# Performance work log

Measured on AMD Instinct MI355X. Metric: run time of the kernel, lower is better.

The kernel has to match this reference:

```python
import jax, jax.numpy as jnp
import numpy as np

B, N, C = 4, 2047, 1024
H = 16
D = C // H  # head_dim = 64
SCALE = D ** -0.5


def setup_inputs() -> dict:
    key = jax.random.key(0)
    ks = jax.random.split(key, 5)
    return {
        "x": jax.random.normal(ks[0], (B, N, C), dtype=jnp.float32),
        "qkv_w": jax.random.normal(ks[1], (3 * C, C), dtype=jnp.float32) * (C ** -0.5),
        "proj_w": jax.random.normal(ks[2], (C, C), dtype=jnp.float32) * (C ** -0.5),
        "proj_b": jax.random.normal(ks[3], (C,), dtype=jnp.float32) * 0.02,
        "bias": jax.random.normal(ks[4], (H, N, N), dtype=jnp.float32) * 0.02,
    }


def reference(x, qkv_w, proj_w, proj_b, bias):
    b, n, c = x.shape
    qkv = (x @ qkv_w.T).reshape(b, n, 3, H, D)
    qkv = jnp.transpose(qkv, (2, 0, 3, 1, 4))
    q, k, v = qkv[0], qkv[1], qkv[2]
    q = q * SCALE
    # scores (B,H,N,N) + additive relative-position bias (H,N,N)
    attn = jnp.einsum('bhnd,bhmd->bhnm', q, k) + bias[None]
    attn = jax.nn.softmax(attn, axis=-1)
    out = jnp.einsum('bhnm,bhmd->bhnd', attn, v)
    out = jnp.transpose(out, (0, 2, 1, 3)).reshape(b, n, c)
    return out @ proj_w.T + proj_b
```

## Files before the change

### kernel.cpp

```cpp
#include <hip/hip_runtime.h>
#include <hip/hip_bf16.h>

typedef __bf16 bf16;
typedef __attribute__((ext_vector_type(8))) __bf16 bf16x8;
typedef __attribute__((ext_vector_type(4))) __bf16 bf16x4;
typedef __attribute__((ext_vector_type(4))) float f32x4;

#define MFMA16(a, b, c) __builtin_amdgcn_mfma_f32_16x16x32_bf16((a), (b), (c), 0, 0, 0)

constexpr int Bb = 4, Nn = 2047, Cc = 1024, Hh = 16, Dd = 64;
constexpr int M_ROWS = Bb * Nn;
constexpr int NPAD = 2048;
constexpr float SCALE = 0.125f;
constexpr float NEG_BIG = -1e30f;

__device__ inline bf16x8 bzero8() {
    bf16x8 v;
    for (int i = 0; i < 8; ++i) v[i] = (bf16)0.0f;
    return v;
}
__device__ inline bf16x8 bones8() {
    bf16x8 v;
    for (int i = 0; i < 8; ++i) v[i] = (bf16)1.0f;
    return v;
}
__device__ inline f32x4 fzero4() {
    f32x4 v = {0.f, 0.f, 0.f, 0.f};
    return v;
}

__device__ __forceinline__ void async_copy16(const void* g, void* l) {
    __builtin_amdgcn_global_load_lds(
        (const __attribute__((address_space(1))) unsigned int*)g,
        (__attribute__((address_space(3))) unsigned int*)l, 16, 0, 0);
}

__global__ __launch_bounds__(256) void cvt3_kernel(
    const float* __restrict__ a, bf16* __restrict__ oa, int na8,
    const float* __restrict__ b, bf16* __restrict__ ob, int nb8,
    const float* __restrict__ c, bf16* __restrict__ oc, int nc8) {
    int i = blockIdx.x * blockDim.x + threadIdx.x;
    const float* src;
    bf16* dst;
    int j = i;
    if (j < na8) {
        src = a; dst = oa;
    } else {
        j -= na8;
        if (j < nb8) {
            src = b; dst = ob;
        } else {
            j -= nb8;
            if (j >= nc8) return;
            src = c; dst = oc;
        }
    }
    float4 x0 = ((const float4*)src)[2 * (size_t)j];
    float4 x1 = ((const float4*)src)[2 * (size_t)j + 1];
    bf16x8 v;
    v[0] = (bf16)x0.x; v[1] = (bf16)x0.y; v[2] = (bf16)x0.z; v[3] = (bf16)x0.w;
    v[4] = (bf16)x1.x; v[5] = (bf16)x1.y; v[6] = (bf16)x1.z; v[7] = (bf16)x1.w;
    *(bf16x8*)(dst + 8 * (size_t)j) = v;
}

__global__ __launch_bounds__(256) void transpose_v_kernel(
    const bf16* __restrict__ vd, bf16* __restrict__ vtd) {
    __shared__ bf16 t[64 * 72];
    const int bh = blockIdx.x, nt = blockIdx.y;
    const int tid = threadIdx.x;
    const bf16* src = vd + (size_t)bh * Nn * Dd;
    bf16* dst = vtd + (size_t)bh * Dd * NPAD;
    int c = tid;
    for (int it = 0; it < 2; ++it, c += 256) {
        int row = c >> 3, d8 = (c & 7) * 8;
        int gn = nt * 64 + row;
        bf16x8 v = bzero8();
        if (gn < Nn) v = *(const bf16x8*)(src + (size_t)gn * Dd + d8);
        *(bf16x8*)(t + row * 72 + d8) = v;
    }
    __syncthreads();
    c = tid;
    for (int it = 0; it < 2; ++it, c += 256) {
        int d = c >> 3, j8 = (c & 7) * 8;
        bf16x8 v;
        for (int k = 0; k < 8; ++k) v[k] = t[(j8 + k) * 72 + d];
        *(bf16x8*)(dst + (size_t)d * NPAD + nt * 64 + j8) = v;
    }
}

template <int NOUT, int MODE>
__global__ __launch_bounds__(256, 2) void gemm_kernel(
    const bf16* __restrict__ A, const bf16* __restrict__ W,
    const float* __restrict__ pb, bf16* __restrict__ qd, bf16* __restrict__ kd,
    bf16* __restrict__ vd, float* __restrict__ outd) {
    constexpr int Kdim = 1024;
    __shared__ bf16 As[128 * 32];
    __shared__ bf16 Bs[128 * 32];

    const int tid = threadIdx.x;
    const int wave = tid >> 6, lane = tid & 63;
    const int quad = lane >> 4, l16 = lane & 15;
    const int m0 = blockIdx.y * 128;
    const int n0 = blockIdx.x * 128;
    const int wm = (wave >> 1) * 64, wn = (wave & 1) * 64;

    const int dma_r = lane >> 2;
    const int dma_k = (lane & 3) * 8;

    f32x4 acc[4][4];
    for (int mi = 0; mi < 4; ++mi)
        for (int ni = 0; ni < 4; ++ni) acc[mi][ni] = fzero4();

    for (int kb = 0; kb < Kdim; kb += 32) {
        __syncthreads();
        for (int i = 0; i < 2; ++i) {
            int g = wave * 2 + i;
            int row = g * 16 + dma_r;
            int gm = m0 + row;
            if (gm > M_ROWS - 1) gm = M_ROWS - 1;
            async_copy16(A + (size_t)gm * Kdim + kb + dma_k, As + g * 16 * 32);
        }
        for (int i = 0; i < 2; ++i) {
            int g = wave * 2 + i;
            int row = g * 16 + dma_r;
            async_copy16(W + (size_t)(n0 + row) * Kdim + kb + dma_k,
                         Bs + g * 16 * 32);
        }
        __syncthreads();

        bf16x8 af[4], bfr[4];
        for (int mi = 0; mi < 4; ++mi)
            af[mi] = *(const bf16x8*)(As + (wm + mi * 16 + l16) * 32 + quad * 8);
        for (int ni = 0; ni < 4; ++ni)
            bfr[ni] = *(const bf16x8*)(Bs + (wn + ni * 16 + l16) * 32 + quad * 8);
        for (int mi = 0; mi < 4; ++mi)
            for (int ni = 0; ni < 4; ++ni)
                acc[mi][ni] = MFMA16(af[mi], bfr[ni], acc[mi][ni]);
    }

    for (int mi = 0; mi < 4; ++mi) {
        for (int r = 0; r < 4; ++r) {
            int gm = m0 + wm + mi * 16 + quad * 4 + r;
            if (gm >= M_ROWS) continue;
            int bb = gm / Nn;
            int nn = gm - bb * Nn;
            for (int ni = 0; ni < 4; ++ni) {
                int gn = n0 + wn + ni * 16 + l16;
                float val = acc[mi][ni][r];
                if (MODE == 0) {
                    int which = gn >> 10;
                    int hh = (gn >> 6) & 15;
                    int dd = gn & 63;
                    size_t dst = ((size_t)(bb * Hh + hh) * Nn + nn) * Dd + dd;
                    if (which == 0)
                        qd[dst] = (bf16)(val * SCALE);
                    else if (which == 1)
                        kd[dst] = (bf16)val;
                    else
                        vd[dst] = (bf16)val;
                } else {
                    outd[(size_t)gm * NOUT + gn] = val + pb[gn];
                }
            }
        }
    }
}

__global__ __launch_bounds__(256, 4) void attn_kernel(
    const bf16* __restrict__ q, const bf16* __restrict__ kk,
    const bf16* __restrict__ vt, const float* __restrict__ bias,
    bf16* __restrict__ out) {
    __shared__ bf16 Qs[64 * 72];
    __shared__ bf16 Ks[64 * 72];
    __shared__ bf16 VTs[64 * 72];
    __shared__ bf16 Ps[64 * 72];

    const int tid = threadIdx.x;
    const int wave = tid >> 6, lane = tid & 63;
    const int quad = lane >> 4, l16 = lane & 15;
    const int b = blockIdx.x, qt = blockIdx.y, h = blockIdx.z;
    const int q0 = qt * 64;
    const int wq0 = wave * 16;

    const size_t head_off = (size_t)(b * Hh + h) * Nn * Dd;
    const bf16* qh = q + head_off;
    const bf16* kh = kk + head_off;
    const bf16* vth = vt + (size_t)(b * Hh + h) * Dd * NPAD;

    int gq_lane = q0 + wq0 + l16;
    if (gq_lane > Nn - 1) gq_lane = Nn - 1;
    const float* brow = bias + ((size_t)h * Nn + gq_lane) * Nn;

    {
        int c = tid;
        for (int it = 0; it < 2; ++it, c += 256) {
            int row = c >> 3, d8 = (c & 7) * 8;
            bf16x8 vq = bzero8();
            int gq = q0 + row;
            if (gq < Nn) vq = *(const bf16x8*)(qh + (size_t)gq * Dd + d8);
            *(bf16x8*)(Qs + row * 72 + d8) = vq;
        }
    }
    __syncthreads();
    const bf16x8 bq0 = *(const bf16x8*)(Qs + (wq0 + l16) * 72 + quad * 8);
    const bf16x8 bq1 = *(const bf16x8*)(Qs + (wq0 + l16) * 72 + 32 + quad * 8);
    const bf16x8 ones = bones8();

    f32x4 acc_o[4];
    for (int nd = 0; nd < 4; ++nd) acc_o[nd] = fzero4();
    f32x4 acc_l = fzero4();
    float m_prev = NEG_BIG;

    for (int t = 0; t < 32; ++t) {
        const int kv0 = t * 64;
        __syncthreads();

        float bv[4][4];
        for (int mi = 0; mi < 4; ++mi)
            for (int r = 0; r < 4; ++r) {
                int kv = kv0 + mi * 16 + quad * 4 + r;
                bv[mi][r] = (kv < Nn) ? brow[kv] : 0.f;
            }

        {
            int c = tid;
            for (int it = 0; it < 2; ++it, c += 256) {
                int row = c >> 3, d8 = (c & 7) * 8;
                int gk = kv0 + row;
                bf16x8 vk = bzero8();
                if (gk < Nn) vk = *(const bf16x8*)(kh + (size_t)gk * Dd + d8);
                *(bf16x8*)(Ks + row * 72 + d8) = vk;
                bf16x8 vv = *(const bf16x8*)(vth + (size_t)row * NPAD + kv0 + d8);
                *(bf16x8*)(VTs + row * 72 + d8) = vv;
            }
        }
        __syncthreads();

        f32x4 sT[4];
        for (int mi = 0; mi < 4; ++mi) sT[mi] = fzero4();
        for (int mi = 0; mi < 4; ++mi) {
            bf16x8 ak0 = *(const bf16x8*)(Ks + (mi * 16 + l16) * 72 + quad * 8);
            bf16x8 ak1 = *(const bf16x8*)(Ks + (mi * 16 + l16) * 72 + 32 + quad * 8);
            sT[mi] = MFMA16(ak0, bq0, sT[mi]);
            sT[mi] = MFMA16(ak1, bq1, sT[mi]);
        }

        float s[4][4];
        for (int mi = 0; mi < 4; ++mi)
            for (int r = 0; r < 4; ++r) {
                int kv = kv0 + mi * 16 + quad * 4 + r;
                s[mi][r] = (kv < Nn) ? sT[mi][r] + bv[mi][r] : NEG_BIG;
            }

        float mx = s[0][0];
        for (int mi = 0; mi < 4; ++mi)
            for (int r = 0; r < 4; ++r) mx = fmaxf(mx, s[mi][r]);
        mx = fmaxf(mx, __shfl_xor(mx, 16));
        mx = fmaxf(mx, __shfl_xor(mx, 32));
        float mnew = fmaxf(m_prev, mx);
        float alpha_col = __expf(m_prev - mnew);
        m_prev = mnew;

        for (int mi = 0; mi < 4; ++mi) {
            bf16x4 pv;
            for (int r = 0; r < 4; ++r)
                pv[r] = (bf16)__expf(s[mi][r] - mnew);
            *(bf16x4*)(Ps + (wq0 + l16) * 72 + mi * 16 + quad * 4) = pv;
        }

        float ar[4];
        for (int r = 0; r < 4; ++r) ar[r] = __shfl(alpha_col, quad * 4 + r);
        for (int nd = 0; nd < 4; ++nd)
            for (int r = 0; r < 4; ++r) acc_o[nd][r] *= ar[r];
        for (int r = 0; r < 4; ++r) acc_l[r] *= ar[r];

        bf16x8 ap0 = *(const bf16x8*)(Ps + (wq0 + l16) * 72 + quad * 8);
        bf16x8 ap1 = *(const bf16x8*)(Ps + (wq0 + l16) * 72 + 32 + quad * 8);
        for (int nd = 0; nd < 4; ++nd) {
            bf16x8 bv0 = *(const bf16x8*)(VTs + (nd * 16 + l16) * 72 + quad * 8);
            bf16x8 bv1 = *(const bf16x8*)(VTs + (nd * 16 + l16) * 72 + 32 + quad * 8);
            acc_o[nd] = MFMA16(ap0, bv0, acc_o[nd]);
            acc_o[nd] = MFMA16(ap1, bv1, acc_o[nd]);
        }
        acc_l = MFMA16(ap0, ones, acc_l);
        acc_l = MFMA16(ap1, ones, acc_l);
    }

    for (int nd = 0; nd < 4; ++nd) {
        for (int r = 0; r < 4; ++r) {
            int gq = q0 + wq0 + quad * 4 + r;
            if (gq >= Nn) continue;
            float val = acc_o[nd][r] / acc_l[r];
            out[((size_t)b * Nn + gq) * Cc + h * 64 + nd * 16 + l16] = (bf16)val;
        }
    }
}

extern "C" void kernel_launch(void* const* d_in, const int* in_sizes, int n_in,
                              void* d_out, int out_size, void* d_ws,
                              size_t ws_size, hipStream_t stream) {
    const float* x = (const float*)d_in[0];
    const float* qkv_w = (const float*)d_in[1];
    const float* proj_w = (const float*)d_in[2];
    const float* proj_b = (const float*)d_in[3];
    const float* bias = (const float*)d_in[4];
    float* out = (float*)d_out;

    const size_t per = (size_t)Bb * Hh * Nn * Dd;
    const size_t nx = (size_t)M_ROWS * Cc;
    const size_t nqw = (size_t)3 * Cc * Cc;
    const size_t npw = (size_t)Cc * Cc;

    bf16* qkvwb = (bf16*)d_ws;
    bf16* projwb = qkvwb + nqw;
    bf16* qd = projwb + npw;
    bf16* kd = qd + per;
    bf16* vd = kd + per;
    bf16* ao = vd + per;
    bf16* xb = ao + nx;
    bf16* vtd = ao + nx;

    {
        int na8 = (int)(nx / 8), nb8 = (int)(nqw / 8), nc8 = (int)(npw / 8);
        int tot = na8 + nb8 + nc8;
        cvt3_kernel<<<(tot + 255) / 256, 256, 0, stream>>>(
            x, xb, na8, qkv_w, qkvwb, nb8, proj_w, projwb, nc8);
    }
    gemm_kernel<3072, 0><<<dim3(24, 64), 256, 0, stream>>>(
        xb, qkvwb, nullptr, qd, kd, vd, nullptr);
    transpose_v_kernel<<<dim3(64, 32), 256, 0, stream>>>(vd, vtd);
    attn_kernel<<<dim3(4, 32, 16), 256, 0, stream>>>(qd, kd, vtd, bias, ao);
    gemm_kernel<1024, 1><<<dim3(8, 64), 256, 0, stream>>>(
        ao, projwb, proj_b, nullptr, nullptr, nullptr, out);
}
```

Baseline: 690.4 us.

## Prefetch next K/V and bias tiles into registers, remap blocks across XCDs

The attention kernel now loads the next tile's K, V^T and bias rows into registers while the current tile computes, then writes them to shared memory at the start of the next iteration. The bias loads become float4 vector loads, with a guarded path for the last tile. The grid is flattened and remapped so the four batches sharing one (head, q-tile) land on the same XCD, which lets them reuse bias data in L2. MFMA sections are wrapped in s_setprio, at the cost of more live registers that may reduce occupancy.

```diff
diff --git a/kernel.cpp b/kernel.cpp
--- a/kernel.cpp
+++ b/kernel.cpp
@@ -178,7 +178,15 @@
     const int tid = threadIdx.x;
     const int wave = tid >> 6, lane = tid & 63;
     const int quad = lane >> 4, l16 = lane & 15;
-    const int b = blockIdx.x, qt = blockIdx.y, h = blockIdx.z;
+
+    const int flat = blockIdx.x;
+    const int xcd = flat & 7;
+    const int sidx = flat >> 3;
+    const int pair = xcd * 64 + (sidx >> 2);
+    const int b = sidx & 3;
+    const int qt = pair & 31;
+    const int h = pair >> 5;
+
     const int q0 = qt * 64;
     const int wq0 = wave * 16;
 
@@ -190,6 +198,9 @@
     int gq_lane = q0 + wq0 + l16;
     if (gq_lane > Nn - 1) gq_lane = Nn - 1;
     const float* brow = bias + ((size_t)h * Nn + gq_lane) * Nn;
+
+    const int srow = tid >> 3;
+    const int sd8 = (tid & 7) * 8;
 
     {
         int c = tid;
@@ -206,6 +217,41 @@
     const bf16x8 bq1 = *(const bf16x8*)(Qs + (wq0 + l16) * 72 + 32 + quad * 8);
     const bf16x8 ones = bones8();
 
+    bf16x8 pk0, pk1, pv0, pv1;
+    float4 bp0, bp1, bp2, bp3;
+
+    auto issue_kv = [&](int kvn) {
+        int g0 = kvn + srow, g1 = kvn + srow + 32;
+        pk0 = bzero8();
+        pk1 = bzero8();
+        if (g0 < Nn) pk0 = *(const bf16x8*)(kh + (size_t)g0 * Dd + sd8);
+        if (g1 < Nn) pk1 = *(const bf16x8*)(kh + (size_t)g1 * Dd + sd8);
+        pv0 = *(const bf16x8*)(vth + (size_t)srow * NPAD + kvn + sd8);
+        pv1 = *(const bf16x8*)(vth + (size_t)(srow + 32) * NPAD + kvn + sd8);
+    };
+    auto issue_bias = [&](int tn) {
+        const int kvn = tn * 64;
+        if (tn < 31) {
+            bp0 = *(const float4*)(brow + kvn + 0 * 16 + quad * 4);
+            bp1 = *(const float4*)(brow + kvn + 1 * 16 + quad * 4);
+            bp2 = *(const float4*)(brow + kvn + 2 * 16 + quad * 4);
+            bp3 = *(const float4*)(brow + kvn + 3 * 16 + quad * 4);
+        } else {
+            float4 f[4];
+            for (int mi = 0; mi < 4; ++mi) {
+                int base = kvn + mi * 16 + quad * 4;
+                f[mi].x = (base + 0 < Nn) ? brow[base + 0] : 0.f;
+                f[mi].y = (base + 1 < Nn) ? brow[base + 1] : 0.f;
+                f[mi].z = (base + 2 < Nn) ? brow[base + 2] : 0.f;
+                f[mi].w = (base + 3 < Nn) ? brow[base + 3] : 0.f;
+            }
+            bp0 = f[0]; bp1 = f[1]; bp2 = f[2]; bp3 = f[3];
+        }
+    };
+
+    issue_kv(0);
+    issue_bias(0);
+
     f32x4 acc_o[4];
     for (int nd = 0; nd < 4; ++nd) acc_o[nd] = fzero4();
     f32x4 acc_l = fzero4();
@@ -215,35 +261,34 @@
         const int kv0 = t * 64;
         __syncthreads();
 
+        *(bf16x8*)(Ks + srow * 72 + sd8) = pk0;
+        *(bf16x8*)(Ks + (srow + 32) * 72 + sd8) = pk1;
+        *(bf16x8*)(VTs + srow * 72 + sd8) = pv0;
+        *(bf16x8*)(VTs + (srow + 32) * 72 + sd8) = pv1;
+
         float bv[4][4];
-        for (int mi = 0; mi < 4; ++mi)
-            for (int r = 0; r < 4; ++r) {
-                int kv = kv0 + mi * 16 + quad * 4 + r;
-                bv[mi][r] = (kv < Nn) ? brow[kv] : 0.f;
-            }
-
-        {
-            int c = tid;
-            for (int it = 0; it < 2; ++it, c += 256) {
-                int row = c >> 3, d8 = (c & 7) * 8;
-                int gk = kv0 + row;
-                bf16x8 vk = bzero8();
-                if (gk < Nn) vk = *(const bf16x8*)(kh + (size_t)gk * Dd + d8);
-                *(bf16x8*)(Ks + row * 72 + d8) = vk;
-                bf16x8 vv = *(const bf16x8*)(vth + (size_t)row * NPAD + kv0 + d8);
-                *(bf16x8*)(VTs + row * 72 + d8) = vv;
-            }
-        }
+        bv[0][0] = bp0.x; bv[0][1] = bp0.y; bv[0][2] = bp0.z; bv[0][3] = bp0.w;
+        bv[1][0] = bp1.x; bv[1][1] = bp1.y; bv[1][2] = bp1.z; bv[1][3] = bp1.w;
+        bv[2][0] = bp2.x; bv[2][1] = bp2.y; bv[2][2] = bp2.z; bv[2][3] = bp2.w;
+        bv[3][0] = bp3.x; bv[3][1] = bp3.y; bv[3][2] = bp3.z; bv[3][3] = bp3.w;
+
         __syncthreads();
+
+        if (t < 31) {
+            issue_kv(kv0 + 64);
+            issue_bias(t + 1);
+        }
 
         f32x4 sT[4];
         for (int mi = 0; mi < 4; ++mi) sT[mi] = fzero4();
+        __builtin_amdgcn_s_setprio(1);
         for (int mi = 0; mi < 4; ++mi) {
             bf16x8 ak0 = *(const bf16x8*)(Ks + (mi * 16 + l16) * 72 + quad * 8);
             bf16x8 ak1 = *(const bf16x8*)(Ks + (mi * 16 + l16) * 72 + 32 + quad * 8);
             sT[mi] = MFMA16(ak0, bq0, sT[mi]);
             sT[mi] = MFMA16(ak1, bq1, sT[mi]);
         }
+        __builtin_amdgcn_s_setprio(0);
 
         float s[4][4];
         for (int mi = 0; mi < 4; ++mi)
@@ -276,6 +321,7 @@
 
         bf16x8 ap0 = *(const bf16x8*)(Ps + (wq0 + l16) * 72 + quad * 8);
         bf16x8 ap1 = *(const bf16x8*)(Ps + (wq0 + l16) * 72 + 32 + quad * 8);
+        __builtin_amdgcn_s_setprio(1);
         for (int nd = 0; nd < 4; ++nd) {
             bf16x8 bv0 = *(const bf16x8*)(VTs + (nd * 16 + l16) * 72 + quad * 8);
             bf16x8 bv1 = *(const bf16x8*)(VTs + (nd * 16 + l16) * 72 + 32 + quad * 8);
@@ -284,6 +330,7 @@
         }
         acc_l = MFMA16(ap0, ones, acc_l);
         acc_l = MFMA16(ap1, ones, acc_l);
+        __builtin_amdgcn_s_setprio(0);
     }
 
     for (int nd = 0; nd < 4; ++nd) {
@@ -329,7 +376,7 @@
     gemm_kernel<3072, 0><<<dim3(24, 64), 256, 0, stream>>>(
         xb, qkvwb, nullptr, qd, kd, vd, nullptr);
     transpose_v_kernel<<<dim3(64, 32), 256, 0, stream>>>(vd, vtd);
-    attn_kernel<<<dim3(4, 32, 16), 256, 0, stream>>>(qd, kd, vtd, bias, ao);
+    attn_kernel<<<dim3(2048), 256, 0, stream>>>(qd, kd, vtd, bias, ao);
     gemm_kernel<1024, 1><<<dim3(8, 64), 256, 0, stream>>>(
         ao, projwb, proj_b, nullptr, nullptr, nullptr, out);
 }
```

Result: faster. 633.6 us (-8.2%).
